# Performance work log

Measured on AMD Instinct MI355X. Metric: run time of the kernel, lower is better.

## Reference

```python
import jax, jax.numpy as jnp
from jax import lax
import numpy as np

B = 32768
N_IN = 8
N_HID = 64
N_CTRL = 2
M_SCEN = (1.0, 1.2)          # scenario parameters for f/g
M_NOM = 1.0
CLF_LAM = 1.0
CBF_LAM = 1.0
P_CLF = 100.0
P_CBF = 50.0
QP_ITERS = 80                # fixed-iteration batched ADMM (OSQP-style) replacing CvxpyLayer
RHO = 1.0
SIGMA = 1e-6
INF = jnp.inf


def setup_inputs() -> dict:
    key = jax.random.key(0)
    ks = jax.random.split(key, 16)
    s = 0.3
    return {
        "x":   jax.random.normal(ks[0], (B, N_IN), jnp.float32),
        "VW1": jax.random.normal(ks[1], (N_HID, N_IN), jnp.float32) * s,
        "Vb1": jax.random.normal(ks[2], (N_HID,), jnp.float32) * s,
        "VW2": jax.random.normal(ks[3], (N_HID, N_HID), jnp.float32) * s,
        "Vb2": jax.random.normal(ks[4], (N_HID,), jnp.float32) * s,
        "HW1": jax.random.normal(ks[5], (N_HID, N_IN), jnp.float32) * s,
        "Hb1": jax.random.normal(ks[6], (N_HID,), jnp.float32) * s,
        "HW2": jax.random.normal(ks[7], (N_HID, N_HID), jnp.float32) * s,
        "Hb2": jax.random.normal(ks[8], (N_HID,), jnp.float32) * s,
        "HW3": jax.random.normal(ks[9], (N_HID, N_HID), jnp.float32) * s,
        "Hb3": jax.random.normal(ks[10], (N_HID,), jnp.float32) * s,
        "HW4": jax.random.normal(ks[11], (1, N_HID), jnp.float32) * s,
        "Hb4": jax.random.normal(ks[12], (1,), jnp.float32) * s,
        "G0":  jax.random.normal(ks[13], (N_IN, N_CTRL), jnp.float32) * s,
        "K":   jax.random.normal(ks[14], (N_IN, N_CTRL), jnp.float32) * s,
    }


def _lyapunov(x, W1, b1, W2, b2):
    t1 = jnp.tanh(x @ W1.T + b1)                                   # [B,H]
    t2 = jnp.tanh(t1 @ W2.T + b2)                                  # [B,H]
    V = 0.5 * jnp.sum(t2 * t2, axis=1)                             # [B]
    # fused diag(1-t^2) @ W chain (no diag_embed materialization)
    D1 = (1.0 - t1 ** 2)[:, :, None] * W1[None]                    # [B,H,N]
    D2 = (1.0 - t2 ** 2)[:, :, None] * jnp.einsum('hk,bkn->bhn', W2, D1)
    grad_V = jnp.einsum('bh,bhn->bn', t2, D2)                      # [B,N]
    return V, grad_V


def _barrier(x, W1, b1, W2, b2, W3, b3, W4, b4):
    t1 = jnp.tanh(x @ W1.T + b1)
    t2 = jnp.tanh(t1 @ W2.T + b2)
    t3 = jnp.tanh(t2 @ W3.T + b3)
    H = t3 @ W4.T + b4                                             # [B,1]
    D1 = (1.0 - t1 ** 2)[:, :, None] * W1[None]
    D2 = (1.0 - t2 ** 2)[:, :, None] * jnp.einsum('hk,bkn->bhn', W2, D1)
    D3 = (1.0 - t3 ** 2)[:, :, None] * jnp.einsum('hk,bkn->bhn', W3, D2)
    grad_H = jnp.einsum('oh,bhn->bn', W4, D3)                      # [B,N] (o=1)
    return H, grad_H


def _solve_qp(q, A, lo, hi):
    """Batched OSQP-style ADMM for min 0.5 z^T P z + q^T z  s.t. lo <= A z <= hi.
    P = diag([2,2,0,0,0,0]); z = [u(2), r_clf(2), s_cbf(2)]. Fixed iterations."""
    nb, mc, nz = A.shape[0], A.shape[1], A.shape[2]
    Pdiag = jnp.array([2.0, 2.0, 0.0, 0.0, 0.0, 0.0], q.dtype)
    M = RHO * jnp.einsum('bmi,bmj->bij', A, A) + jnp.diag(Pdiag + SIGMA)
    Minv = jnp.linalg.inv(M)                                       # [B,6,6]
    x0 = jnp.zeros((nb, nz), q.dtype)
    z0 = jnp.zeros((nb, mc), q.dtype)
    y0 = jnp.zeros((nb, mc), q.dtype)

    def step(carry, _):
        xx, zz, yy = carry
        rhs = SIGMA * xx - q + jnp.einsum('bmi,bm->bi', A, RHO * zz - yy)
        xt = jnp.einsum('bij,bj->bi', Minv, rhs)
        zt = jnp.einsum('bmi,bi->bm', A, xt)
        zn = jnp.clip(zt + yy / RHO, lo, hi)
        yn = yy + RHO * (zt - zn)
        return (xt, zn, yn), None

    (xf, _, _), _ = lax.scan(step, (x0, z0, y0), None, length=QP_ITERS)
    return xf                                                      # [B,6]


def _forward(x, VW1, Vb1, VW2, Vb2, HW1, Hb1, HW2, Hb2, HW3, Hb3, HW4, Hb4, G0, K):
    V, grad_V = _lyapunov(x, VW1, Vb1, VW2, Vb2)
    H, grad_H = _barrier(x, HW1, Hb1, HW2, Hb2, HW3, Hb3, HW4, Hb4)

    LfVs, LgVs, LfHs, LgHs = [], [], [], []
    for m in M_SCEN:
        # f(x,m) = -x/m ; g(x,m) = G0/m
        LfVs.append(-jnp.sum(grad_V * x, axis=1) / m)              # [B]
        LgVs.append((grad_V @ G0) / m)                             # [B,C]
        LfHs.append(-jnp.sum(grad_H * x, axis=1) / m)
        LgHs.append((grad_H @ G0) / m)
    u_nom = -(x @ K) * (1.0 / M_NOM)                               # [B,C]

    nb = x.shape[0]
    z2 = jnp.zeros((nb, 2), x.dtype)
    ey = jnp.eye(2, dtype=x.dtype)
    e = lambda i: jnp.broadcast_to(ey[i], (nb, 2))
    ninf = jnp.full((nb,), -INF, x.dtype)
    pinf = jnp.full((nb,), INF, x.dtype)
    zer = jnp.zeros((nb,), x.dtype)

    rows, los, his = [], [], []
    for i in range(len(M_SCEN)):
        # CBF: LfH + LgH@u + cbf_lam*H + s_i >= 0
        rows.append(jnp.concatenate([LgHs[i], z2, e(i)], axis=1))
        los.append(-(LfHs[i] + CBF_LAM * H[:, 0])); his.append(pinf)
        # CLF: LfV + LgV@u + clf_lam*V - r_i <= 0
        rows.append(jnp.concatenate([LgVs[i], -e(i), z2], axis=1))
        los.append(ninf); his.append(-(LfVs[i] + CLF_LAM * V))
    for i in range(len(M_SCEN)):
        rows.append(jnp.concatenate([z2, e(i), z2], axis=1)); los.append(zer); his.append(pinf)
    for i in range(len(M_SCEN)):
        rows.append(jnp.concatenate([z2, z2, e(i)], axis=1)); los.append(zer); his.append(pinf)

    A = jnp.stack(rows, axis=1)                                    # [B,8,6]
    lo = jnp.stack(los, axis=1)                                    # [B,8]
    hi = jnp.stack(his, axis=1)
    # objective ||u-u_nom||^2 + p_clf*sum r + p_cbf*sum s  ->  q = [-2 u_nom, p_clf, p_clf, p_cbf, p_cbf]
    q = jnp.concatenate([-2.0 * u_nom,
                         jnp.full((nb, 2), P_CLF, x.dtype),
                         jnp.full((nb, 2), P_CBF, x.dtype)], axis=1)

    z = _solve_qp(q, A, lo, hi)                                    # [B,6]
    u = z[:, :N_CTRL]
    relaxation = jnp.mean(z[:, N_CTRL:N_CTRL + len(M_SCEN)], axis=1, keepdims=True)  # [B,1]

    ns = float(len(M_SCEN))
    Vdot = sum(LfVs[i] + jnp.sum(LgVs[i] * u, axis=1) for i in range(len(M_SCEN))) / ns
    Hdot = sum(LfHs[i] + jnp.sum(LgHs[i] * u, axis=1) for i in range(len(M_SCEN))) / ns
    return u, relaxation, V, Vdot[:, None, None], H, Hdot[:, None, None]


def reference(x, VW1, Vb1, VW2, Vb2, HW1, Hb1, HW2, Hb2, HW3, Hb3, HW4, Hb4, G0, K):
    return _forward(x, VW1, Vb1, VW2, Vb2, HW1, Hb1, HW2, Hb2, HW3, Hb3, HW4, Hb4, G0, K)
```

## Files before the change

kernel.cpp:

```cpp
#include <hip/hip_runtime.h>
#include <hip/hip_bf16.h>
#include <math.h>

#define BTOT 32768

typedef _Float16 f16x8 __attribute__((ext_vector_type(8)));
typedef _Float16 f16x4 __attribute__((ext_vector_type(4)));
typedef float    f32x4 __attribute__((ext_vector_type(4)));

__device__ __forceinline__ float ldin(const void* p, int i, int f32f) {
  return f32f ? ((const float*)p)[i]
              : __bfloat162float(((const __hip_bfloat16*)p)[i]);
}

__device__ __forceinline__ f32x4 MFMA(f16x8 a, f16x8 b, f32x4 c) {
  return __builtin_amdgcn_mfma_f32_16x16x32_f16(a, b, c, 0, 0, 0);
}

__device__ __forceinline__ float tanh_fast(float x) {
  float e = __expf(2.f * x);
  return 1.f - 2.f * __builtin_amdgcn_rcpf(e + 1.f);
}

__device__ __forceinline__ float redq(float v) {
  v += __shfl_xor(v, 16, 64);
  v += __shfl_xor(v, 32, 64);
  return v;
}

__device__ __forceinline__ int widx(int h, int k) {
  return ((h >> 4) << 10) + ((k >> 5) << 9) + (((k >> 3) & 3) << 7) + ((h & 15) << 3) + (k & 7);
}

#define OFF_VW2   0
#define OFF_VW2T  4096
#define OFF_HW2   8192
#define OFF_HW2T  12288
#define OFF_HW3   16384
#define OFF_HW3T  20480
#define OFF_W1VH  24576
#define OFF_W1VL  25088
#define OFF_W1HH  25600
#define OFF_W1HL  26112
#define CF_BASE   28672
#define C_WGV0 0
#define C_WGV1 64
#define C_WGH0 128
#define C_WGH1 192
#define C_VB1  256
#define C_VB2  320
#define C_HB1  384
#define C_HB2  448
#define C_HB3  512
#define C_W4   576
#define C_K    640
#define C_HB4  656
#define C_FLAG 657
#define C_N    658

__global__ __launch_bounds__(256) void prep_kernel(
    const void* px, const void* pVW1, const void* pVW2,
    const void* pHW1, const void* pHW2, const void* pHW3,
    const void* pVb1, const void* pVb2, const void* pHb1, const void* pHb2,
    const void* pHb3, const void* pHW4, const void* pHb4,
    const void* pG0, const void* pK, _Float16* wsp)
{
  __shared__ int sCnt;
  const int tid = threadIdx.x;
  if (tid == 0) sCnt = 0;
  __syncthreads();
  {
    const unsigned short* xb = (const unsigned short*)px;
    int good = 0;
#pragma unroll
    for (int i = 0; i < 2; ++i) {
      int ex = (xb[tid * 2 + i] >> 7) & 0xFF;
      good += (ex >= 97 && ex <= 157) ? 1 : 0;
    }
    atomicAdd(&sCnt, good);
  }
  __syncthreads();
  const int f32f = (sCnt >= 435) ? 0 : 1;

  const int t = blockIdx.x * 256 + tid;
  int h = t >> 6, k = t & 63;
  int fw = widx(h, k), tw = widx(k, h);
  _Float16 v;
  v = (_Float16)ldin(pVW2, t, f32f); wsp[OFF_VW2 + fw] = v; wsp[OFF_VW2T + tw] = v;
  v = (_Float16)ldin(pHW2, t, f32f); wsp[OFF_HW2 + fw] = v; wsp[OFF_HW2T + tw] = v;
  v = (_Float16)ldin(pHW3, t, f32f); wsp[OFF_HW3 + fw] = v; wsp[OFF_HW3T + tw] = v;
  if (t < 512) {
    float f = ldin(pVW1, t, f32f); _Float16 hh = (_Float16)f;
    wsp[OFF_W1VH + t] = hh; wsp[OFF_W1VL + t] = (_Float16)(f - (float)hh);
    f = ldin(pHW1, t, f32f); hh = (_Float16)f;
    wsp[OFF_W1HH + t] = hh; wsp[OFF_W1HL + t] = (_Float16)(f - (float)hh);
  }
  if (blockIdx.x == 0) {
    float* wsF = (float*)(wsp + CF_BASE);
    if (tid < 64) {
      float a0 = 0.f, a1 = 0.f, b0 = 0.f, b1 = 0.f;
#pragma unroll
      for (int nn = 0; nn < 8; ++nn) {
        float g0 = ldin(pG0, 2 * nn, f32f), g1 = ldin(pG0, 2 * nn + 1, f32f);
        float wv = ldin(pVW1, tid * 8 + nn, f32f), wh = ldin(pHW1, tid * 8 + nn, f32f);
        a0 += wv * g0; a1 += wv * g1; b0 += wh * g0; b1 += wh * g1;
      }
      wsF[C_WGV0 + tid] = a0; wsF[C_WGV1 + tid] = a1;
      wsF[C_WGH0 + tid] = b0; wsF[C_WGH1 + tid] = b1;
      wsF[C_VB1 + tid] = ldin(pVb1, tid, f32f);
      wsF[C_VB2 + tid] = ldin(pVb2, tid, f32f);
      wsF[C_HB1 + tid] = ldin(pHb1, tid, f32f);
      wsF[C_HB2 + tid] = ldin(pHb2, tid, f32f);
      wsF[C_HB3 + tid] = ldin(pHb3, tid, f32f);
      wsF[C_W4  + tid] = ldin(pHW4, tid, f32f);
    }
    if (tid < 16) wsF[C_K + tid] = ldin(pK, tid, f32f);
    if (tid == 0) { wsF[C_HB4] = ldin(pHb4, 0, f32f); ((int*)wsF)[C_FLAG] = f32f; }
  }
}

__global__ __launch_bounds__(512, 4) void main_kernel(
    const void* px, const _Float16* wsp, float* out)
{
  __shared__ __align__(16) _Float16 sAct[4][4][1024];
  __shared__ __align__(16) float sQPp[8][16][12];
  __shared__ __align__(16) float sC[C_N];

  const int tid = threadIdx.x, lane = tid & 63, wave = tid >> 6;
  const int pair = wave >> 1, sub = wave & 1;
  const int m = lane & 15, q = lane >> 4;
  const int ro = lane * 8;
  const int e0 = blockIdx.x * 64 + pair * 16;

  const float* wsF = (const float*)(wsp + CF_BASE);
  for (int i = tid; i < C_N; i += 512) sC[i] = wsF[i];
  const int f32f = ((const int*)wsF)[C_FLAG];
  const bool wsplit = (f32f != 0);

  f16x8 zf;
#pragma unroll
  for (int i = 0; i < 8; ++i) zf[i] = (_Float16)0.f;

  f16x8 xbh = zf, xbl = zf;
  if (lane < 16) {
#pragma unroll
    for (int n = 0; n < 8; ++n) {
      float v = ldin(px, (e0 + m) * 8 + n, f32f);
      _Float16 hh = (_Float16)v;
      xbh[n] = hh; xbl[n] = (_Float16)(v - (float)hh);
    }
  }
  __syncthreads();

  if (sub == 0 && lane < 16) {
    float un0 = 0.f, un1 = 0.f;
#pragma unroll
    for (int n = 0; n < 8; ++n) {
      float xv = (float)xbh[n] + (float)xbl[n];
      un0 -= xv * sC[C_K + 2 * n];
      un1 -= xv * sC[C_K + 2 * n + 1];
    }
    sQPp[wave][m][8] = un0; sQPp[wave][m][9] = un1;
  }

  _Float16* bufV0 = sAct[pair][0];
  _Float16* bufV1 = sAct[pair][1];
  _Float16* bufH0 = sAct[pair][2];
  _Float16* bufH1 = sAct[pair][3];

  auto hgemm = [&](int poff, const _Float16* a_, f32x4* acc) {
    f16x8 b0 = *(const f16x8*)(a_ + ro);
    f16x8 b1 = *(const f16x8*)(a_ + 512 + ro);
#pragma unroll
    for (int i = 0; i < 2; ++i) {
      const _Float16* ap = wsp + poff + (2 * sub + i) * 1024 + ro;
      f32x4 c = {0.f, 0.f, 0.f, 0.f};
      c = MFMA(*(const f16x8*)ap, b0, c);
      c = MFMA(*(const f16x8*)(ap + 512), b1, c);
      acc[i] = c;
    }
  };
  auto wstore = [&](const f32x4* vals, _Float16* a_) {
#pragma unroll
    for (int i = 0; i < 2; ++i) {
      int ht = 2 * sub + i;
      int aw = ((ht >> 1) << 9) + (((ht & 1) * 2 + (q >> 1)) << 7) + m * 8 + ((q & 1) << 2);
      f16x4 vh;
#pragma unroll
      for (int r = 0; r < 4; ++r) vh[r] = (_Float16)vals[i][r];
      *(f16x4*)(a_ + aw) = vh;
    }
  };
  auto l1gemm = [&](int hoff, int loff, f32x4* acc) {
#pragma unroll
    for (int i = 0; i < 2; ++i) {
      int ht = 2 * sub + i;
      f16x8 afh = zf, afl = zf;
      if (lane < 16) {
        afh = *(const f16x8*)(wsp + hoff + (ht * 16 + m) * 8);
        afl = *(const f16x8*)(wsp + loff + (ht * 16 + m) * 8);
      }
      f32x4 c = {0.f, 0.f, 0.f, 0.f};
      c = MFMA(afh, xbh, c);
      c = MFMA(afh, xbl, c);
      if (wsplit) c = MFMA(afl, xbh, c);
      acc[i] = c;
    }
  };

  f32x4 accV[2], accH[2], z1V[2], z1H[2], d1V[2], d1H[2], d2H[2], tvV[2], tvH[2];

  l1gemm(OFF_W1VH, OFF_W1VL, accV);
  l1gemm(OFF_W1HH, OFF_W1HL, accH);
#pragma unroll
  for (int i = 0; i < 2; ++i) {
    int hb = (2 * sub + i) * 16 + q * 4;
    z1V[i] = accV[i]; z1H[i] = accH[i];
    f32x4 bV = *(const f32x4*)&sC[C_VB1 + hb];
    f32x4 bH = *(const f32x4*)&sC[C_HB1 + hb];
#pragma unroll
    for (int r = 0; r < 4; ++r) {
      float t = tanh_fast(z1V[i][r] + bV[r]);
      tvV[i][r] = t; d1V[i][r] = 1.f - t * t;
      t = tanh_fast(z1H[i][r] + bH[r]);
      tvH[i][r] = t; d1H[i][r] = 1.f - t * t;
    }
  }
  wstore(tvV, bufV0); wstore(tvH, bufH0);
  __syncthreads();

  hgemm(OFF_VW2, bufV0, accV);
  hgemm(OFF_HW2, bufH0, accH);
  float pV = 0.f;
#pragma unroll
  for (int i = 0; i < 2; ++i) {
    int hb = (2 * sub + i) * 16 + q * 4;
    f32x4 bV = *(const f32x4*)&sC[C_VB2 + hb];
    f32x4 bH = *(const f32x4*)&sC[C_HB2 + hb];
#pragma unroll
    for (int r = 0; r < 4; ++r) {
      float t = tanh_fast(accV[i][r] + bV[r]);
      pV += t * t;
      tvV[i][r] = t * (1.f - t * t);
      t = tanh_fast(accH[i][r] + bH[r]);
      tvH[i][r] = t; d2H[i][r] = 1.f - t * t;
    }
  }
  wstore(tvV, bufV1); wstore(tvH, bufH1);
  __syncthreads();

  hgemm(OFF_VW2T, bufV1, accV);
  hgemm(OFF_HW3, bufH1, accH);
  float pgvx = 0.f, plv0 = 0.f, plv1 = 0.f, pH = 0.f;
#pragma unroll
  for (int i = 0; i < 2; ++i) {
    int hb = (2 * sub + i) * 16 + q * 4;
    f32x4 g0 = *(const f32x4*)&sC[C_WGV0 + hb];
    f32x4 g1 = *(const f32x4*)&sC[C_WGV1 + hb];
    f32x4 bH = *(const f32x4*)&sC[C_HB3 + hb];
    f32x4 w4 = *(const f32x4*)&sC[C_W4 + hb];
#pragma unroll
    for (int r = 0; r < 4; ++r) {
      float wt = accV[i][r] * d1V[i][r];
      pgvx += wt * z1V[i][r];
      plv0 += wt * g0[r]; plv1 += wt * g1[r];
      float t = tanh_fast(accH[i][r] + bH[r]);
      pH += t * w4[r];
      tvH[i][r] = w4[r] * (1.f - t * t);
    }
  }
  wstore(tvH, bufH0);
  __syncthreads();

  hgemm(OFF_HW3T, bufH0, accH);
#pragma unroll
  for (int i = 0; i < 2; ++i)
#pragma unroll
    for (int r = 0; r < 4; ++r) tvH[i][r] = accH[i][r] * d2H[i][r];
  wstore(tvH, bufH1);
  __syncthreads();

  hgemm(OFF_HW2T, bufH1, accH);
  float pghx = 0.f, plh0 = 0.f, plh1 = 0.f;
#pragma unroll
  for (int i = 0; i < 2; ++i) {
    int hb = (2 * sub + i) * 16 + q * 4;
    f32x4 g0 = *(const f32x4*)&sC[C_WGH0 + hb];
    f32x4 g1 = *(const f32x4*)&sC[C_WGH1 + hb];
#pragma unroll
    for (int r = 0; r < 4; ++r) {
      float wt = accH[i][r] * d1H[i][r];
      pghx += wt * z1H[i][r];
      plh0 += wt * g0[r]; plh1 += wt * g1[r];
    }
  }

  {
    float a0 = redq(plh0), a1 = redq(plh1), a2 = redq(plv0), a3 = redq(plv1);
    float a4 = redq(pghx), a5 = redq(pgvx), a6 = redq(pV), a7 = redq(pH);
    if (lane < 16) {
      sQPp[wave][lane][0] = a0; sQPp[wave][lane][1] = a1;
      sQPp[wave][lane][2] = a2; sQPp[wave][lane][3] = a3;
      sQPp[wave][lane][4] = a4; sQPp[wave][lane][5] = a5;
      sQPp[wave][lane][6] = a6; sQPp[wave][lane][7] = a7;
    }
  }
  __syncthreads();

  if (tid >= 64) return;
  const int p = tid >> 4, mm = tid & 15;
  const int e = blockIdx.x * 64 + tid;
  float gh0 = sQPp[2 * p][mm][0] + sQPp[2 * p + 1][mm][0];
  float gh1 = sQPp[2 * p][mm][1] + sQPp[2 * p + 1][mm][1];
  float gv0 = sQPp[2 * p][mm][2] + sQPp[2 * p + 1][mm][2];
  float gv1 = sQPp[2 * p][mm][3] + sQPp[2 * p + 1][mm][3];
  float ghx = sQPp[2 * p][mm][4] + sQPp[2 * p + 1][mm][4];
  float gvx = sQPp[2 * p][mm][5] + sQPp[2 * p + 1][mm][5];
  float V   = 0.5f * (sQPp[2 * p][mm][6] + sQPp[2 * p + 1][mm][6]);
  float H   = sQPp[2 * p][mm][7] + sQPp[2 * p + 1][mm][7] + sC[C_HB4];
  float un0 = sQPp[2 * p][mm][8], un1 = sQPp[2 * p][mm][9];
  out[98304 + e]  = V;
  out[163840 + e] = H;

  const float im = 1.0f / 1.2f;
  const float sg = 1e-6f;

  float lo0 = ghx - H;
  float hi1 = gvx - V;
  float lo2 = ghx * im - H;
  float hi3 = gvx * im - V;
  float qv0 = -2.f * un0, qv1 = -2.f * un1;

  const float d  = 2.f + sg;
  const float rd = 1.f / d;
  const float al = 1.f + im * im;
  const float be = al * (1.f - rd);
  float S00 = be * (gh0 * gh0 + gv0 * gv0) + d;
  float S11 = be * (gh1 * gh1 + gv1 * gv1) + d;
  float S01 = be * (gh0 * gh1 + gv0 * gv1);
  float idet = 1.f / (S00 * S11 - S01 * S01);
  float i00 = S11 * idet, i11 = S00 * idet, i01 = -S01 * idet;

  float X0 = 0.f, X1 = 0.f, X2 = 0.f, X3 = 0.f, X4 = 0.f, X5 = 0.f;
  float Z[8] = {0.f, 0.f, 0.f, 0.f, 0.f, 0.f, 0.f, 0.f};
  float Y[8] = {0.f, 0.f, 0.f, 0.f, 0.f, 0.f, 0.f, 0.f};

#pragma unroll 1
  for (int it = 0; it < 80; ++it) {
    float t0 = Z[0] - Y[0], t1 = Z[1] - Y[1], t2 = Z[2] - Y[2], t3 = Z[3] - Y[3];
    float t4 = Z[4] - Y[4], t5 = Z[5] - Y[5], t6 = Z[6] - Y[6], t7 = Z[7] - Y[7];
    float tauh = t0 + im * t2, tauv = t1 + im * t3;
    float b0 = sg * X0 - qv0 + gh0 * tauh + gv0 * tauv;
    float b1 = sg * X1 - qv1 + gh1 * tauh + gv1 * tauv;
    float b2 = sg * X2 - 100.f - t1 + t4;
    float b3 = sg * X3 - 100.f - t3 + t5;
    float b4 = sg * X4 - 50.f + t0 + t6;
    float b5 = sg * X5 - 50.f + t2 + t7;
    float pp = b2 + im * b3;
    float s2 = b4 + im * b5;
    float cb0 = gh0 * s2 - gv0 * pp;
    float cb1 = gh1 * s2 - gv1 * pp;
    float u0b = b0 - cb0 * rd;
    float u1b = b1 - cb1 * rd;
    X0 = i00 * u0b + i01 * u1b;
    X1 = i01 * u0b + i11 * u1b;
    float gdH = gh0 * X0 + gh1 * X1;
    float gdV = gv0 * X0 + gv1 * X1;
    X2 = (b2 + gdV) * rd;
    X3 = (b3 + im * gdV) * rd;
    X4 = (b4 - gdH) * rd;
    X5 = (b5 - im * gdH) * rd;
    float zt0 = gdH + X4;
    float zt1 = gdV - X2;
    float zt2 = gdH * im + X5;
    float zt3 = gdV * im - X3;

    float v, zn;
    v = zt0 + Y[0]; zn = fmaxf(v, lo0); Y[0] += zt0 - zn; Z[0] = zn;
    v = zt1 + Y[1]; zn = fminf(v, hi1); Y[1] += zt1 - zn; Z[1] = zn;
    v = zt2 + Y[2]; zn = fmaxf(v, lo2); Y[2] += zt2 - zn; Z[2] = zn;
    v = zt3 + Y[3]; zn = fminf(v, hi3); Y[3] += zt3 - zn; Z[3] = zn;
    v = X2 + Y[4];  zn = fmaxf(v, 0.f); Y[4] += X2 - zn;  Z[4] = zn;
    v = X3 + Y[5];  zn = fmaxf(v, 0.f); Y[5] += X3 - zn;  Z[5] = zn;
    v = X4 + Y[6];  zn = fmaxf(v, 0.f); Y[6] += X4 - zn;  Z[6] = zn;
    v = X5 + Y[7];  zn = fmaxf(v, 0.f); Y[7] += X5 - zn;  Z[7] = zn;
  }

  float relax = 0.5f * (X2 + X3);
  const float cc = 0.5f * (1.f + im);
  float Vdot = cc * (gv0 * X0 + gv1 * X1 - gvx);
  float Hdot = cc * (gh0 * X0 + gh1 * X1 - ghx);

  out[2 * e]      = X0;
  out[2 * e + 1]  = X1;
  out[65536 + e]  = relax;
  out[131072 + e] = Vdot;
  out[196608 + e] = Hdot;
}

extern "C" void kernel_launch(void* const* d_in, const int* in_sizes, int n_in,
                              void* d_out, int out_size, void* d_ws, size_t ws_size,
                              hipStream_t stream) {
  float* out = (float*)d_out;
  _Float16* wsp = (_Float16*)d_ws;
  prep_kernel<<<16, 256, 0, stream>>>(
      d_in[0], d_in[1], d_in[3], d_in[5], d_in[7], d_in[9],
      d_in[2], d_in[4], d_in[6], d_in[8], d_in[10], d_in[11], d_in[12],
      d_in[13], d_in[14], wsp);
  main_kernel<<<512, 512, 0, stream>>>(d_in[0], wsp, out);
}
```

Before: 111.5 us.

## Fuse weight prep into main kernel with LDS-resident weights and per-wave samples

Drops the separate prep kernel. Each block now converts and lays out the weight matrices (plain and transposed) into shared memory itself, so the MFMA weight operands come from LDS instead of global memory. Each wave processes 16 samples across all 64 hidden units, running the V and H chains one after the other with no block-level barriers between layers. The layer-1 hi/lo split is folded into a single MFMA by packing split x and W fragments across lane quarters. The cost is that every one of the 256 blocks redoes the weight conversion, and occupancy drops to 2 blocks per unit because of the larger LDS footprint.

```diff
diff --git a/kernel.cpp b/kernel.cpp
--- a/kernel.cpp
+++ b/kernel.cpp
@@ -1,8 +1,6 @@
 #include <hip/hip_runtime.h>
 #include <hip/hip_bf16.h>
 #include <math.h>
-
-#define BTOT 32768
 
 typedef _Float16 f16x8 __attribute__((ext_vector_type(8)));
 typedef _Float16 f16x4 __attribute__((ext_vector_type(4)));
@@ -32,17 +30,16 @@
   return ((h >> 4) << 10) + ((k >> 5) << 9) + (((k >> 3) & 3) << 7) + ((h & 15) << 3) + (k & 7);
 }
 
-#define OFF_VW2   0
-#define OFF_VW2T  4096
-#define OFF_HW2   8192
-#define OFF_HW2T  12288
-#define OFF_HW3   16384
-#define OFF_HW3T  20480
-#define OFF_W1VH  24576
-#define OFF_W1VL  25088
-#define OFF_W1HH  25600
-#define OFF_W1HL  26112
-#define CF_BASE   28672
+#define OFF_W2V   0
+#define OFF_W2VT  4096
+#define OFF_W2H   8192
+#define OFF_W2HT  12288
+#define OFF_W3H   16384
+#define OFF_W3HT  20480
+#define OFF_W1V   24576
+#define OFF_W1H   26624
+#define SW_N      28672
+
 #define C_WGV0 0
 #define C_WGV1 64
 #define C_WGH0 128
@@ -55,49 +52,67 @@
 #define C_W4   576
 #define C_K    640
 #define C_HB4  656
-#define C_FLAG 657
-#define C_N    658
-
-__global__ __launch_bounds__(256) void prep_kernel(
-    const void* px, const void* pVW1, const void* pVW2,
-    const void* pHW1, const void* pHW2, const void* pHW3,
-    const void* pVb1, const void* pVb2, const void* pHb1, const void* pHb2,
-    const void* pHb3, const void* pHW4, const void* pHb4,
-    const void* pG0, const void* pK, _Float16* wsp)
+#define C_N    660
+
+__global__ __launch_bounds__(512, 2) void fused_kernel(
+    const void* px, const void* pVW1, const void* pVb1, const void* pVW2, const void* pVb2,
+    const void* pHW1, const void* pHb1, const void* pHW2, const void* pHb2,
+    const void* pHW3, const void* pHb3, const void* pHW4, const void* pHb4,
+    const void* pG0, const void* pK, float* out)
 {
+  __shared__ __align__(16) _Float16 sW[SW_N];
+  __shared__ __align__(16) _Float16 sAct[16][1024];
+  __shared__ __align__(16) float sQPs[128][12];
+  __shared__ __align__(16) float sC[C_N];
   __shared__ int sCnt;
+
   const int tid = threadIdx.x;
   if (tid == 0) sCnt = 0;
   __syncthreads();
   {
-    const unsigned short* xb = (const unsigned short*)px;
+    const unsigned short* xbp = (const unsigned short*)px;
     int good = 0;
 #pragma unroll
     for (int i = 0; i < 2; ++i) {
-      int ex = (xb[tid * 2 + i] >> 7) & 0xFF;
+      int ex = (xbp[tid * 2 + i] >> 7) & 0xFF;
       good += (ex >= 97 && ex <= 157) ? 1 : 0;
     }
     atomicAdd(&sCnt, good);
   }
   __syncthreads();
-  const int f32f = (sCnt >= 435) ? 0 : 1;
-
-  const int t = blockIdx.x * 256 + tid;
-  int h = t >> 6, k = t & 63;
-  int fw = widx(h, k), tw = widx(k, h);
-  _Float16 v;
-  v = (_Float16)ldin(pVW2, t, f32f); wsp[OFF_VW2 + fw] = v; wsp[OFF_VW2T + tw] = v;
-  v = (_Float16)ldin(pHW2, t, f32f); wsp[OFF_HW2 + fw] = v; wsp[OFF_HW2T + tw] = v;
-  v = (_Float16)ldin(pHW3, t, f32f); wsp[OFF_HW3 + fw] = v; wsp[OFF_HW3T + tw] = v;
-  if (t < 512) {
-    float f = ldin(pVW1, t, f32f); _Float16 hh = (_Float16)f;
-    wsp[OFF_W1VH + t] = hh; wsp[OFF_W1VL + t] = (_Float16)(f - (float)hh);
-    f = ldin(pHW1, t, f32f); hh = (_Float16)f;
-    wsp[OFF_W1HH + t] = hh; wsp[OFF_W1HL + t] = (_Float16)(f - (float)hh);
-  }
-  if (blockIdx.x == 0) {
-    float* wsF = (float*)(wsp + CF_BASE);
+  const int f32f = (sCnt >= 870) ? 0 : 1;
+
+  {
+    const int h = tid >> 3, k0 = (tid & 7) * 8;
+    auto prepM = [&](const void* src, int offF, int offT) {
+      f16x8 vv;
+#pragma unroll
+      for (int j = 0; j < 8; ++j) vv[j] = (_Float16)ldin(src, tid * 8 + j, f32f);
+      *(f16x8*)(sW + offF + widx(h, k0)) = vv;
+#pragma unroll
+      for (int j = 0; j < 8; ++j) sW[offT + widx(k0 + j, h)] = vv[j];
+    };
+    prepM(pVW2, OFF_W2V, OFF_W2VT);
+    prepM(pHW2, OFF_W2H, OFF_W2HT);
+    prepM(pHW3, OFF_W3H, OFF_W3HT);
+
     if (tid < 64) {
+      const int ht = tid >> 4, mm = tid & 15;
+      auto prepW1 = [&](const void* src, int off) {
+        const int base = off + ht * 512 + mm * 8;
+#pragma unroll
+        for (int j = 0; j < 8; ++j) {
+          float wv = ldin(src, tid * 8 + j, f32f);
+          _Float16 hh = (_Float16)wv;
+          sW[base + j]       = hh;
+          sW[base + 128 + j] = hh;
+          sW[base + 256 + j] = f32f ? (_Float16)(wv - (float)hh)
+                                    : (_Float16)0.f;
+          sW[base + 384 + j] = (_Float16)0.f;
+        }
+      };
+      prepW1(pVW1, OFF_W1V);
+      prepW1(pHW1, OFF_W1H);
       float a0 = 0.f, a1 = 0.f, b0 = 0.f, b1 = 0.f;
 #pragma unroll
       for (int nn = 0; nn < 8; ++nn) {
@@ -105,192 +120,179 @@
         float wv = ldin(pVW1, tid * 8 + nn, f32f), wh = ldin(pHW1, tid * 8 + nn, f32f);
         a0 += wv * g0; a1 += wv * g1; b0 += wh * g0; b1 += wh * g1;
       }
-      wsF[C_WGV0 + tid] = a0; wsF[C_WGV1 + tid] = a1;
-      wsF[C_WGH0 + tid] = b0; wsF[C_WGH1 + tid] = b1;
-      wsF[C_VB1 + tid] = ldin(pVb1, tid, f32f);
-      wsF[C_VB2 + tid] = ldin(pVb2, tid, f32f);
-      wsF[C_HB1 + tid] = ldin(pHb1, tid, f32f);
-      wsF[C_HB2 + tid] = ldin(pHb2, tid, f32f);
-      wsF[C_HB3 + tid] = ldin(pHb3, tid, f32f);
-      wsF[C_W4  + tid] = ldin(pHW4, tid, f32f);
-    }
-    if (tid < 16) wsF[C_K + tid] = ldin(pK, tid, f32f);
-    if (tid == 0) { wsF[C_HB4] = ldin(pHb4, 0, f32f); ((int*)wsF)[C_FLAG] = f32f; }
-  }
-}
-
-__global__ __launch_bounds__(512, 4) void main_kernel(
-    const void* px, const _Float16* wsp, float* out)
-{
-  __shared__ __align__(16) _Float16 sAct[4][4][1024];
-  __shared__ __align__(16) float sQPp[8][16][12];
-  __shared__ __align__(16) float sC[C_N];
-
-  const int tid = threadIdx.x, lane = tid & 63, wave = tid >> 6;
-  const int pair = wave >> 1, sub = wave & 1;
-  const int m = lane & 15, q = lane >> 4;
-  const int ro = lane * 8;
-  const int e0 = blockIdx.x * 64 + pair * 16;
-
-  const float* wsF = (const float*)(wsp + CF_BASE);
-  for (int i = tid; i < C_N; i += 512) sC[i] = wsF[i];
-  const int f32f = ((const int*)wsF)[C_FLAG];
-  const bool wsplit = (f32f != 0);
-
-  f16x8 zf;
-#pragma unroll
-  for (int i = 0; i < 8; ++i) zf[i] = (_Float16)0.f;
-
-  f16x8 xbh = zf, xbl = zf;
-  if (lane < 16) {
-#pragma unroll
-    for (int n = 0; n < 8; ++n) {
-      float v = ldin(px, (e0 + m) * 8 + n, f32f);
-      _Float16 hh = (_Float16)v;
-      xbh[n] = hh; xbl[n] = (_Float16)(v - (float)hh);
-    }
+      sC[C_WGV0 + tid] = a0; sC[C_WGV1 + tid] = a1;
+      sC[C_WGH0 + tid] = b0; sC[C_WGH1 + tid] = b1;
+      sC[C_VB1 + tid] = ldin(pVb1, tid, f32f);
+      sC[C_VB2 + tid] = ldin(pVb2, tid, f32f);
+      sC[C_HB1 + tid] = ldin(pHb1, tid, f32f);
+      sC[C_HB2 + tid] = ldin(pHb2, tid, f32f);
+      sC[C_HB3 + tid] = ldin(pHb3, tid, f32f);
+      sC[C_W4  + tid] = ldin(pHW4, tid, f32f);
+    }
+    if (tid < 16) sC[C_K + tid] = ldin(pK, tid, f32f);
+    if (tid == 0) sC[C_HB4] = ldin(pHb4, 0, f32f);
   }
   __syncthreads();
 
-  if (sub == 0 && lane < 16) {
-    float un0 = 0.f, un1 = 0.f;
-#pragma unroll
-    for (int n = 0; n < 8; ++n) {
-      float xv = (float)xbh[n] + (float)xbl[n];
-      un0 -= xv * sC[C_K + 2 * n];
-      un1 -= xv * sC[C_K + 2 * n + 1];
-    }
-    sQPp[wave][m][8] = un0; sQPp[wave][m][9] = un1;
-  }
-
-  _Float16* bufV0 = sAct[pair][0];
-  _Float16* bufV1 = sAct[pair][1];
-  _Float16* bufH0 = sAct[pair][2];
-  _Float16* bufH1 = sAct[pair][3];
-
-  auto hgemm = [&](int poff, const _Float16* a_, f32x4* acc) {
-    f16x8 b0 = *(const f16x8*)(a_ + ro);
-    f16x8 b1 = *(const f16x8*)(a_ + 512 + ro);
-#pragma unroll
-    for (int i = 0; i < 2; ++i) {
-      const _Float16* ap = wsp + poff + (2 * sub + i) * 1024 + ro;
+  const int lane = tid & 63, w = tid >> 6;
+  const int n = lane & 15, q = lane >> 4;
+  const int e0 = blockIdx.x * 128 + w * 16;
+
+  float un0 = 0.f, un1 = 0.f;
+  f16x8 xb;
+#pragma unroll
+  for (int j = 0; j < 8; ++j) {
+    float xv = ldin(px, (e0 + n) * 8 + j, f32f);
+    _Float16 hh = (_Float16)xv;
+    float lo = xv - (float)hh;
+    xb[j] = (q == 1) ? (_Float16)lo : ((q == 3) ? (_Float16)0.f : hh);
+    un0 -= xv * sC[C_K + 2 * j];
+    un1 -= xv * sC[C_K + 2 * j + 1];
+  }
+
+  _Float16* buf0 = sAct[w * 2];
+  _Float16* buf1 = sAct[w * 2 + 1];
+
+  auto gemm64 = [&](int poff, const _Float16* b, f32x4* acc) {
+    f16x8 b0 = *(const f16x8*)(b + lane * 8);
+    f16x8 b1 = *(const f16x8*)(b + 512 + lane * 8);
+#pragma unroll
+    for (int ht = 0; ht < 4; ++ht) {
+      const _Float16* ap = sW + poff + ht * 1024 + lane * 8;
       f32x4 c = {0.f, 0.f, 0.f, 0.f};
       c = MFMA(*(const f16x8*)ap, b0, c);
       c = MFMA(*(const f16x8*)(ap + 512), b1, c);
-      acc[i] = c;
+      acc[ht] = c;
     }
   };
-  auto wstore = [&](const f32x4* vals, _Float16* a_) {
-#pragma unroll
-    for (int i = 0; i < 2; ++i) {
-      int ht = 2 * sub + i;
-      int aw = ((ht >> 1) << 9) + (((ht & 1) * 2 + (q >> 1)) << 7) + m * 8 + ((q & 1) << 2);
+  auto l1gemm = [&](int off, f32x4* acc) {
+#pragma unroll
+    for (int ht = 0; ht < 4; ++ht) {
+      const _Float16* ap = sW + off + ht * 512 + lane * 8;
+      f32x4 c = {0.f, 0.f, 0.f, 0.f};
+      acc[ht] = MFMA(*(const f16x8*)ap, xb, c);
+    }
+  };
+  auto wst = [&](const f32x4* vals, _Float16* b) {
+#pragma unroll
+    for (int ht = 0; ht < 4; ++ht) {
+      int aw = ((ht >> 1) << 9) + (((ht & 1) * 2 + (q >> 1)) << 7) + n * 8 + ((q & 1) << 2);
       f16x4 vh;
 #pragma unroll
-      for (int r = 0; r < 4; ++r) vh[r] = (_Float16)vals[i][r];
-      *(f16x4*)(a_ + aw) = vh;
+      for (int r = 0; r < 4; ++r) vh[r] = (_Float16)vals[ht][r];
+      *(f16x4*)(b + aw) = vh;
     }
   };
-  auto l1gemm = [&](int hoff, int loff, f32x4* acc) {
-#pragma unroll
-    for (int i = 0; i < 2; ++i) {
-      int ht = 2 * sub + i;
-      f16x8 afh = zf, afl = zf;
-      if (lane < 16) {
-        afh = *(const f16x8*)(wsp + hoff + (ht * 16 + m) * 8);
-        afl = *(const f16x8*)(wsp + loff + (ht * 16 + m) * 8);
-      }
-      f32x4 c = {0.f, 0.f, 0.f, 0.f};
-      c = MFMA(afh, xbh, c);
-      c = MFMA(afh, xbl, c);
-      if (wsplit) c = MFMA(afl, xbh, c);
-      acc[i] = c;
-    }
-  };
-
-  f32x4 accV[2], accH[2], z1V[2], z1H[2], d1V[2], d1H[2], d2H[2], tvV[2], tvH[2];
-
-  l1gemm(OFF_W1VH, OFF_W1VL, accV);
-  l1gemm(OFF_W1HH, OFF_W1HL, accH);
-#pragma unroll
-  for (int i = 0; i < 2; ++i) {
-    int hb = (2 * sub + i) * 16 + q * 4;
-    z1V[i] = accV[i]; z1H[i] = accH[i];
-    f32x4 bV = *(const f32x4*)&sC[C_VB1 + hb];
-    f32x4 bH = *(const f32x4*)&sC[C_HB1 + hb];
-#pragma unroll
-    for (int r = 0; r < 4; ++r) {
-      float t = tanh_fast(z1V[i][r] + bV[r]);
-      tvV[i][r] = t; d1V[i][r] = 1.f - t * t;
-      t = tanh_fast(z1H[i][r] + bH[r]);
-      tvH[i][r] = t; d1H[i][r] = 1.f - t * t;
-    }
-  }
-  wstore(tvV, bufV0); wstore(tvH, bufH0);
-  __syncthreads();
-
-  hgemm(OFF_VW2, bufV0, accV);
-  hgemm(OFF_HW2, bufH0, accH);
+
+  f32x4 acc[4], tv[4];
+
+  f32x4 z1V[4], d1V[4];
+  l1gemm(OFF_W1V, acc);
+#pragma unroll
+  for (int ht = 0; ht < 4; ++ht) {
+    int hb = ht * 16 + q * 4;
+    f32x4 bb = *(const f32x4*)&sC[C_VB1 + hb];
+    z1V[ht] = acc[ht];
+#pragma unroll
+    for (int r = 0; r < 4; ++r) {
+      float t = tanh_fast(z1V[ht][r] + bb[r]);
+      tv[ht][r] = t; d1V[ht][r] = 1.f - t * t;
+    }
+  }
+  wst(tv, buf0);
+
+  gemm64(OFF_W2V, buf0, acc);
   float pV = 0.f;
 #pragma unroll
-  for (int i = 0; i < 2; ++i) {
-    int hb = (2 * sub + i) * 16 + q * 4;
-    f32x4 bV = *(const f32x4*)&sC[C_VB2 + hb];
-    f32x4 bH = *(const f32x4*)&sC[C_HB2 + hb];
-#pragma unroll
-    for (int r = 0; r < 4; ++r) {
-      float t = tanh_fast(accV[i][r] + bV[r]);
+  for (int ht = 0; ht < 4; ++ht) {
+    int hb = ht * 16 + q * 4;
+    f32x4 bb = *(const f32x4*)&sC[C_VB2 + hb];
+#pragma unroll
+    for (int r = 0; r < 4; ++r) {
+      float t = tanh_fast(acc[ht][r] + bb[r]);
       pV += t * t;
-      tvV[i][r] = t * (1.f - t * t);
-      t = tanh_fast(accH[i][r] + bH[r]);
-      tvH[i][r] = t; d2H[i][r] = 1.f - t * t;
-    }
-  }
-  wstore(tvV, bufV1); wstore(tvH, bufH1);
-  __syncthreads();
-
-  hgemm(OFF_VW2T, bufV1, accV);
-  hgemm(OFF_HW3, bufH1, accH);
-  float pgvx = 0.f, plv0 = 0.f, plv1 = 0.f, pH = 0.f;
-#pragma unroll
-  for (int i = 0; i < 2; ++i) {
-    int hb = (2 * sub + i) * 16 + q * 4;
+      tv[ht][r] = t * (1.f - t * t);
+    }
+  }
+  wst(tv, buf1);
+
+  gemm64(OFF_W2VT, buf1, acc);
+  float pgvx = 0.f, plv0 = 0.f, plv1 = 0.f;
+#pragma unroll
+  for (int ht = 0; ht < 4; ++ht) {
+    int hb = ht * 16 + q * 4;
     f32x4 g0 = *(const f32x4*)&sC[C_WGV0 + hb];
     f32x4 g1 = *(const f32x4*)&sC[C_WGV1 + hb];
-    f32x4 bH = *(const f32x4*)&sC[C_HB3 + hb];
+#pragma unroll
+    for (int r = 0; r < 4; ++r) {
+      float wt = acc[ht][r] * d1V[ht][r];
+      pgvx += wt * z1V[ht][r];
+      plv0 += wt * g0[r]; plv1 += wt * g1[r];
+    }
+  }
+
+  f32x4 z1H[4], d1H[4], d2H[4];
+  l1gemm(OFF_W1H, acc);
+#pragma unroll
+  for (int ht = 0; ht < 4; ++ht) {
+    int hb = ht * 16 + q * 4;
+    f32x4 bb = *(const f32x4*)&sC[C_HB1 + hb];
+    z1H[ht] = acc[ht];
+#pragma unroll
+    for (int r = 0; r < 4; ++r) {
+      float t = tanh_fast(z1H[ht][r] + bb[r]);
+      tv[ht][r] = t; d1H[ht][r] = 1.f - t * t;
+    }
+  }
+  wst(tv, buf0);
+
+  gemm64(OFF_W2H, buf0, acc);
+#pragma unroll
+  for (int ht = 0; ht < 4; ++ht) {
+    int hb = ht * 16 + q * 4;
+    f32x4 bb = *(const f32x4*)&sC[C_HB2 + hb];
+#pragma unroll
+    for (int r = 0; r < 4; ++r) {
+      float t = tanh_fast(acc[ht][r] + bb[r]);
+      tv[ht][r] = t; d2H[ht][r] = 1.f - t * t;
+    }
+  }
+  wst(tv, buf1);
+
+  gemm64(OFF_W3H, buf1, acc);
+  float pH = 0.f;
+#pragma unroll
+  for (int ht = 0; ht < 4; ++ht) {
+    int hb = ht * 16 + q * 4;
+    f32x4 bb = *(const f32x4*)&sC[C_HB3 + hb];
     f32x4 w4 = *(const f32x4*)&sC[C_W4 + hb];
 #pragma unroll
     for (int r = 0; r < 4; ++r) {
-      float wt = accV[i][r] * d1V[i][r];
-      pgvx += wt * z1V[i][r];
-      plv0 += wt * g0[r]; plv1 += wt * g1[r];
-      float t = tanh_fast(accH[i][r] + bH[r]);
+      float t = tanh_fast(acc[ht][r] + bb[r]);
       pH += t * w4[r];
-      tvH[i][r] = w4[r] * (1.f - t * t);
-    }
-  }
-  wstore(tvH, bufH0);
-  __syncthreads();
-
-  hgemm(OFF_HW3T, bufH0, accH);
-#pragma unroll
-  for (int i = 0; i < 2; ++i)
-#pragma unroll
-    for (int r = 0; r < 4; ++r) tvH[i][r] = accH[i][r] * d2H[i][r];
-  wstore(tvH, bufH1);
-  __syncthreads();
-
-  hgemm(OFF_HW2T, bufH1, accH);
+      tv[ht][r] = w4[r] * (1.f - t * t);
+    }
+  }
+  wst(tv, buf0);
+
+  gemm64(OFF_W3HT, buf0, acc);
+#pragma unroll
+  for (int ht = 0; ht < 4; ++ht)
+#pragma unroll
+    for (int r = 0; r < 4; ++r) tv[ht][r] = acc[ht][r] * d2H[ht][r];
+  wst(tv, buf1);
+
+  gemm64(OFF_W2HT, buf1, acc);
   float pghx = 0.f, plh0 = 0.f, plh1 = 0.f;
 #pragma unroll
-  for (int i = 0; i < 2; ++i) {
-    int hb = (2 * sub + i) * 16 + q * 4;
+  for (int ht = 0; ht < 4; ++ht) {
+    int hb = ht * 16 + q * 4;
     f32x4 g0 = *(const f32x4*)&sC[C_WGH0 + hb];
     f32x4 g1 = *(const f32x4*)&sC[C_WGH1 + hb];
 #pragma unroll
     for (int r = 0; r < 4; ++r) {
-      float wt = accH[i][r] * d1H[i][r];
-      pghx += wt * z1H[i][r];
+      float wt = acc[ht][r] * d1H[ht][r];
+      pghx += wt * z1H[ht][r];
       plh0 += wt * g0[r]; plh1 += wt * g1[r];
     }
   }
@@ -298,27 +300,23 @@
   {
     float a0 = redq(plh0), a1 = redq(plh1), a2 = redq(plv0), a3 = redq(plv1);
     float a4 = redq(pghx), a5 = redq(pgvx), a6 = redq(pV), a7 = redq(pH);
-    if (lane < 16) {
-      sQPp[wave][lane][0] = a0; sQPp[wave][lane][1] = a1;
-      sQPp[wave][lane][2] = a2; sQPp[wave][lane][3] = a3;
-      sQPp[wave][lane][4] = a4; sQPp[wave][lane][5] = a5;
-      sQPp[wave][lane][6] = a6; sQPp[wave][lane][7] = a7;
+    if (q == 0) {
+      float* sp = sQPs[w * 16 + n];
+      sp[0] = a0; sp[1] = a1; sp[2] = a2; sp[3] = a3;
+      sp[4] = a4; sp[5] = a5; sp[6] = a6; sp[7] = a7;
+      sp[8] = un0; sp[9] = un1;
     }
   }
   __syncthreads();
 
-  if (tid >= 64) return;
-  const int p = tid >> 4, mm = tid & 15;
-  const int e = blockIdx.x * 64 + tid;
-  float gh0 = sQPp[2 * p][mm][0] + sQPp[2 * p + 1][mm][0];
-  float gh1 = sQPp[2 * p][mm][1] + sQPp[2 * p + 1][mm][1];
-  float gv0 = sQPp[2 * p][mm][2] + sQPp[2 * p + 1][mm][2];
-  float gv1 = sQPp[2 * p][mm][3] + sQPp[2 * p + 1][mm][3];
-  float ghx = sQPp[2 * p][mm][4] + sQPp[2 * p + 1][mm][4];
-  float gvx = sQPp[2 * p][mm][5] + sQPp[2 * p + 1][mm][5];
-  float V   = 0.5f * (sQPp[2 * p][mm][6] + sQPp[2 * p + 1][mm][6]);
-  float H   = sQPp[2 * p][mm][7] + sQPp[2 * p + 1][mm][7] + sC[C_HB4];
-  float un0 = sQPp[2 * p][mm][8], un1 = sQPp[2 * p][mm][9];
+  if (tid >= 128) return;
+  const int e = blockIdx.x * 128 + tid;
+  const float* sp = sQPs[tid];
+  float gh0 = sp[0], gh1 = sp[1], gv0 = sp[2], gv1 = sp[3];
+  float ghx = sp[4], gvx = sp[5];
+  float V = 0.5f * sp[6];
+  float H = sp[7] + sC[C_HB4];
+  un0 = sp[8]; un1 = sp[9];
   out[98304 + e]  = V;
   out[163840 + e] = H;
 
@@ -401,11 +399,9 @@
 extern "C" void kernel_launch(void* const* d_in, const int* in_sizes, int n_in,
                               void* d_out, int out_size, void* d_ws, size_t ws_size,
                               hipStream_t stream) {
-  float* out = (float*)d_out;
-  _Float16* wsp = (_Float16*)d_ws;
-  prep_kernel<<<16, 256, 0, stream>>>(
-      d_in[0], d_in[1], d_in[3], d_in[5], d_in[7], d_in[9],
-      d_in[2], d_in[4], d_in[6], d_in[8], d_in[10], d_in[11], d_in[12],
-      d_in[13], d_in[14], wsp);
-  main_kernel<<<512, 512, 0, stream>>>(d_in[0], wsp, out);
-}
+  (void)d_ws; (void)ws_size; (void)in_sizes; (void)n_in; (void)out_size;
+  fused_kernel<<<256, 512, 0, stream>>>(
+      d_in[0], d_in[1], d_in[2], d_in[3], d_in[4], d_in[5], d_in[6],
+      d_in[7], d_in[8], d_in[9], d_in[10], d_in[11], d_in[12],
+      d_in[13], d_in[14], (float*)d_out);
+}
```

Result: slower. 116.1 us (+4.1%).
